# Optimization experiments

Hardware: AMD Instinct MI355X
Metric: run time of the kernel (lower is better)

The kernel has to match this reference:

```python
import jax, jax.numpy as jnp
import numpy as np


def _norm_adj(edge_index, edge_weights, num_nodes):
    """Faithful port of edge_index2norm_adj: dense scatter + self-loops +
    symmetric degree normalization (deg_inv_sqrt is detached in the original)."""
    row, col = edge_index[0], edge_index[1]
    half = edge_weights * 0.5
    adj = jnp.zeros((num_nodes, num_nodes), dtype=edge_weights.dtype)
    adj = adj.at[row, col].add(half)
    adj = adj.at[col, row].add(half)
    adj = adj + jnp.eye(num_nodes, dtype=adj.dtype)
    deg = adj.sum(axis=1)
    deg_inv_sqrt = jnp.where(deg > 0, jax.lax.rsqrt(deg), 0.0)
    deg_inv_sqrt = jax.lax.stop_gradient(deg_inv_sqrt)  # torch.no_grad + detach
    return deg_inv_sqrt[:, None] * adj * deg_inv_sqrt[None, :]


def setup_inputs() -> dict:
    key = jax.random.key(0)
    k1, k2, k3, k4, k5 = jax.random.split(key, 5)
    N, E, D_IN, D_H, D_OUT = 16384, 524288, 64, 64, 16
    x = jax.random.normal(k1, (N, D_IN), dtype=jnp.float32)
    edge_index = jax.random.randint(k2, (2, E), 0, N, dtype=jnp.int64)
    edge_weights = jax.random.uniform(k3, (E,), dtype=jnp.float32)
    W1 = jax.random.normal(k4, (D_IN, D_H), dtype=jnp.float32) / np.sqrt(D_IN)
    b1 = jnp.zeros((D_H,), dtype=jnp.float32)
    W2 = jax.random.normal(k5, (D_H, D_OUT), dtype=jnp.float32) / np.sqrt(D_H)
    b2 = jnp.zeros((D_OUT,), dtype=jnp.float32)
    return {"x": x, "W1": W1, "b1": b1, "W2": W2, "b2": b2,
            "edge_weights": edge_weights, "edge_index": edge_index}


def reference(x, W1, b1, W2, b2, edge_weights, edge_index):
    num_nodes = x.shape[0]
    A = _norm_adj(edge_index, edge_weights, num_nodes)   # [N, N]
    h = jax.nn.relu(A @ (x @ W1) + b1)                   # GCN layer 1
    out = A @ (h @ W2) + b2                              # GCN layer 2 (logits)
    return out
```

## Files before the change

kernel.cpp:

```cpp
#include <hip/hip_runtime.h>

constexpr int TPB   = 256;
constexpr int NMAX  = 16384;
constexpr int CHUNK = 2048;
constexpr int GBMAX = 1024;
constexpr int STGN  = 12288;
constexpr int RCAP  = 12;



__global__ __launch_bounds__(1024) void k_p1(const int* __restrict__ ei,
    const float* __restrict__ ew, int E, int rsh, int NBe, int GB,
    int* __restrict__ bstartT, int* __restrict__ bcntT, int2* __restrict__ tmp) {
    __shared__ int cnt[256];
    __shared__ int curs[256];
    __shared__ int sc[256];
    __shared__ int2 stg[2 * CHUNK];
    int tid = threadIdx.x;
    int b = blockIdx.x;
    int e0 = b * CHUNK;
    int e1 = min(E, e0 + CHUNK);
    if (tid < NBe) cnt[tid] = 0;
    __syncthreads();
    int ea = e0 + tid, ebg = e0 + 1024 + tid;
    int r0 = 0, c0 = 0, r1 = 0, c1 = 0, w0 = 0, w1 = 0;
    bool va = ea < e1, vb = ebg < e1;
    if (va) { r0 = ei[ea];  c0 = ei[E + ea];  w0 = __float_as_int(0.5f * ew[ea]); }
    if (vb) { r1 = ei[ebg]; c1 = ei[E + ebg]; w1 = __float_as_int(0.5f * ew[ebg]); }
    if (va) { atomicAdd(&cnt[r0 >> rsh], 1); atomicAdd(&cnt[c0 >> rsh], 1); }
    if (vb) { atomicAdd(&cnt[r1 >> rsh], 1); atomicAdd(&cnt[c1 >> rsh], 1); }
    __syncthreads();
    int myc = (tid < NBe) ? cnt[tid] : 0;
    if (tid < NBe) sc[tid] = myc;
    __syncthreads();
    for (int off = 1; off < NBe; off <<= 1) {
        int v = 0;
        if (tid < NBe && tid >= off) v = sc[tid - off];
        __syncthreads();
        if (tid < NBe) sc[tid] += v;
        __syncthreads();
    }
    if (tid < NBe) {
        int excl = sc[tid] - myc;
        curs[tid] = excl;
        bstartT[tid * GB + b] = 2 * e0 + excl;
        bcntT[tid * GB + b] = myc;
    }
    __syncthreads();
    int mask = (1 << rsh) - 1;
    if (va) {
        int p = atomicAdd(&curs[r0 >> rsh], 1);
        stg[p] = make_int2(((r0 & mask) << 20) | c0, w0);
        p = atomicAdd(&curs[c0 >> rsh], 1);
        stg[p] = make_int2(((c0 & mask) << 20) | r0, w0);
    }
    if (vb) {
        int p = atomicAdd(&curs[r1 >> rsh], 1);
        stg[p] = make_int2(((r1 & mask) << 20) | c1, w1);
        p = atomicAdd(&curs[c1 >> rsh], 1);
        stg[p] = make_int2(((c1 & mask) << 20) | r1, w1);
    }
    __syncthreads();
    int tot = 2 * (e1 - e0);
    for (int i = tid; i < tot; i += 1024) tmp[2 * e0 + i] = stg[i];
}

__global__ void k_colsum(const int* __restrict__ bcntT, int GB,
                         int* __restrict__ btot) {
    __shared__ int red[TPB / 64];
    int k = blockIdx.x;
    int s = 0;
    for (int b = threadIdx.x; b < GB; b += TPB) s += bcntT[k * GB + b];
    #pragma unroll
    for (int off = 32; off; off >>= 1) s += __shfl_down(s, off, 64);
    int wv = threadIdx.x >> 6;
    if ((threadIdx.x & 63) == 0) red[wv] = s;
    __syncthreads();
    if (threadIdx.x == 0) {
        int t = 0;
        for (int w = 0; w < TPB / 64; ++w) t += red[w];
        btot[k] = t;
    }
}

__global__ __launch_bounds__(1024) void k_p2(const int2* __restrict__ tmp,
    const int* __restrict__ bstartT, const int* __restrict__ bcntT,
    const int* __restrict__ btot, int GB, int rsh, int N, int NBe, int M,
    int2* __restrict__ ent, int* __restrict__ rowptr, float* __restrict__ dis) {
    __shared__ int sco[256];
    __shared__ int ncnt[64];
    __shared__ int nstart[64];
    __shared__ int ncur[64];
    __shared__ float wsum[64];
    __shared__ int2 stg[STGN];
    int k = blockIdx.x;
    int tid = threadIdx.x;
    int RN = 1 << rsh;
    int n0 = k << rsh;
    const int base = k * GB;

    int grp = tid >> 2, sub = tid & 3;
    int s0 = 0, l0 = 0;
    if (grp < GB) { s0 = bstartT[base + grp]; l0 = bcntT[base + grp]; }
    int2 r[RCAP];
    #pragma unroll
    for (int u = 0; u < RCAP; ++u) {
        int idx = sub + 4 * u;
        if (idx < l0) r[u] = tmp[s0 + idx];
    }

    int bt = (tid < NBe) ? btot[tid] : 0;
    if (tid < 256) sco[tid] = bt;
    if (tid < RN) { ncnt[tid] = 0; wsum[tid] = 0.f; }
    __syncthreads();
    for (int off = 1; off < 256; off <<= 1) {
        int v = 0;
        if (tid < 256 && tid >= off) v = sco[tid - off];
        __syncthreads();
        if (tid < 256) sco[tid] += v;
        __syncthreads();
    }
    int eb = sco[k] - btot[k];
    int tot = btot[k];
    bool useStg = (tot <= STGN);

    #pragma unroll
    for (int u = 0; u < RCAP; ++u)
        if (sub + 4 * u < l0) atomicAdd(&ncnt[r[u].x >> 20], 1);
    for (int idx = sub + 4 * RCAP; idx < l0; idx += 4)
        atomicAdd(&ncnt[tmp[s0 + idx].x >> 20], 1);
    for (int b = grp + 256; b < GB; b += 256) {
        int s = bstartT[base + b], l = bcntT[base + b];
        for (int idx = sub; idx < l; idx += 4)
            atomicAdd(&ncnt[tmp[s + idx].x >> 20], 1);
    }
    __syncthreads();

    int myc = (tid < RN) ? ncnt[tid] : 0;
    if (tid < RN) nstart[tid] = myc;
    __syncthreads();
    for (int off = 1; off < RN; off <<= 1) {
        int v = 0;
        if (tid < RN && tid >= off) v = nstart[tid - off];
        __syncthreads();
        if (tid < RN) nstart[tid] += v;
        __syncthreads();
    }
    if (tid < RN) { nstart[tid] -= myc; ncur[tid] = nstart[tid]; }
    __syncthreads();

    #pragma unroll
    for (int u = 0; u < RCAP; ++u)
        if (sub + 4 * u < l0) {
            int rl = r[u].x >> 20;
            int p = atomicAdd(&ncur[rl], 1);
            int2 v2 = make_int2(r[u].x & 0xFFFFF, r[u].y);
            if (useStg) stg[p] = v2; else ent[eb + p] = v2;
            atomicAdd(&wsum[rl], __int_as_float(r[u].y));
        }
    for (int idx = sub + 4 * RCAP; idx < l0; idx += 4) {
        int2 v = tmp[s0 + idx];
        int rl = v.x >> 20;
        int p = atomicAdd(&ncur[rl], 1);
        int2 v2 = make_int2(v.x & 0xFFFFF, v.y);
        if (useStg) stg[p] = v2; else ent[eb + p] = v2;
        atomicAdd(&wsum[rl], __int_as_float(v.y));
    }
    for (int b = grp + 256; b < GB; b += 256) {
        int s = bstartT[base + b], l = bcntT[base + b];
        for (int idx = sub; idx < l; idx += 4) {
            int2 v = tmp[s + idx];
            int rl = v.x >> 20;
            int p = atomicAdd(&ncur[rl], 1);
            int2 v2 = make_int2(v.x & 0xFFFFF, v.y);
            if (useStg) stg[p] = v2; else ent[eb + p] = v2;
            atomicAdd(&wsum[rl], __int_as_float(v.y));
        }
    }
    __syncthreads();
    if (useStg)
        for (int i = tid; i < tot; i += 1024) ent[eb + i] = stg[i];
    if (tid < RN && n0 + tid < N) {
        rowptr[n0 + tid] = eb + nstart[tid];
        dis[n0 + tid] = rsqrtf(1.f + wsum[tid]);
    }
    if (k == 0 && tid == 0) rowptr[N] = M;
}

__global__ void k_init_fb(float* deg, int* counts, int N) {
    int i = blockIdx.x * TPB + threadIdx.x;
    if (i < N) { deg[i] = 1.0f; counts[i] = 0; }
}
__global__ void k_deg_cnt_fb(const int* __restrict__ ei, const float* __restrict__ ew,
                             float* deg, int* counts, int E) {
    int e = blockIdx.x * TPB + threadIdx.x;
    if (e >= E) return;
    int r = ei[e], c = ei[E + e];
    float hw = 0.5f * ew[e];
    unsafeAtomicAdd(&deg[r], hw);
    unsafeAtomicAdd(&deg[c], hw);
    atomicAdd(&counts[r], 1);
    atomicAdd(&counts[c], 1);
}
__global__ void k_rsqrt_fb(float* degdis, int N) {
    int i = blockIdx.x * TPB + threadIdx.x;
    if (i < N) {
        float d = degdis[i];
        degdis[i] = d > 0.f ? rsqrtf(d) : 0.f;
    }
}
__global__ void k_scan_fb(const int* __restrict__ counts, int* __restrict__ rowptr,
                          int* __restrict__ cursor, int N) {
    __shared__ int partial[TPB];
    int tid = threadIdx.x;
    int chunk = (N + TPB - 1) / TPB;
    int begin = tid * chunk;
    int end = begin + chunk; if (end > N) end = N;
    int s = 0;
    for (int i = begin; i < end; ++i) s += counts[i];
    partial[tid] = s;
    __syncthreads();
    for (int off = 1; off < TPB; off <<= 1) {
        int v = partial[tid];
        int add = (tid >= off) ? partial[tid - off] : 0;
        __syncthreads();
        partial[tid] = v + add;
        __syncthreads();
    }
    int base = (tid == 0) ? 0 : partial[tid - 1];
    for (int i = begin; i < end; ++i) {
        rowptr[i] = base; cursor[i] = base;
        base += counts[i];
    }
    if (tid == TPB - 1) rowptr[N] = base;
}
__global__ void k_fill_fb(const int* __restrict__ ei, const float* __restrict__ ew,
                          int* cursor, int2* __restrict__ ent, int E) {
    int e = blockIdx.x * TPB + threadIdx.x;
    if (e >= E) return;
    int r = ei[e], c = ei[E + e];
    int hw = __float_as_int(0.5f * ew[e]);
    int p1 = atomicAdd(&cursor[r], 1);
    ent[p1] = make_int2(c, hw);
    int p2 = atomicAdd(&cursor[c], 1);
    ent[p2] = make_int2(r, hw);
}

__global__ void k_gemm1(const float* __restrict__ X, const float* __restrict__ W,
                        const float* __restrict__ dis, float* __restrict__ Z, int N) {
    __shared__ float Wl[64 * 64];
    int tid = threadIdx.x;
    #pragma unroll
    for (int i = tid; i < 4096; i += TPB) Wl[i] = W[i];
    __syncthreads();
    int row = blockIdx.x * 4 + (tid >> 6);
    int f = tid & 63;
    if (row >= N) return;
    const float* xr = X + row * 64;
    float s = 0.f;
    #pragma unroll
    for (int k = 0; k < 64; ++k) s = fmaf(xr[k], Wl[k * 64 + f], s);
    Z[row * 64 + f] = dis[row] * s;
}

__global__ __launch_bounds__(TPB) void k_gather1(const float* __restrict__ Z,
    const int* __restrict__ rowptr, const long long* __restrict__ entq,
    const float* __restrict__ dis, const float* __restrict__ bias1,
    const float* __restrict__ W2, float* __restrict__ Z2, int N) {
    constexpr int UN = 16;
    __shared__ float W2l[64 * 16];
    int tid = threadIdx.x;
    #pragma unroll
    for (int i = tid; i < 1024; i += TPB) W2l[i] = W2[i];
    __syncthreads();
    int node = blockIdx.x * 4 + (tid >> 6);
    int f = tid & 63;
    if (node >= N) return;
    int sj0 = __builtin_amdgcn_readfirstlane(rowptr[node]);
    int sj1 = __builtin_amdgcn_readfirstlane(rowptr[node + 1]);
    float acc = Z[node * 64 + f];
    float dn = dis[node];
    for (int jb = sj0; jb < sj1; jb += UN) {
        long long e[UN];
        #pragma unroll
        for (int u = 0; u < UN; ++u) e[u] = entq[jb + u];
        float z[UN];
        #pragma unroll
        for (int u = 0; u < UN; ++u) {
            int nn = (jb + u < sj1) ? (int)e[u] : 0;
            z[u] = Z[nn * 64 + f];
        }
        #pragma unroll
        for (int u = 0; u < UN; ++u) {
            float ww = (jb + u < sj1) ? __int_as_float((int)(e[u] >> 32)) : 0.0f;
            acc = fmaf(ww, z[u], acc);
        }
    }
    float v = fmaf(dn, acc, bias1[f]);
    v = v > 0.f ? v : 0.f;
    int q = f >> 4, j = f & 15;
    float s = 0.f;
    #pragma unroll
    for (int i = 0; i < 16; ++i) {
        float hk = __shfl(v, 16 * q + i);
        s = fmaf(hk, W2l[(16 * q + i) * 16 + j], s);
    }
    s += __shfl_xor(s, 16);
    s += __shfl_xor(s, 32);
    if (f < 16) Z2[node * 16 + f] = dn * s;
}

__global__ __launch_bounds__(TPB) void k_gather2(const float* __restrict__ Z,
    const int* __restrict__ rowptr, const long long* __restrict__ entq,
    const float* __restrict__ dis, const float* __restrict__ bias,
    float* __restrict__ out, int N) {
    constexpr int UN = 4;
    int node = blockIdx.x * 4 + (threadIdx.x >> 6);
    int lane = threadIdx.x & 63;
    int g = lane >> 4;
    int f = lane & 15;
    if (node >= N) return;
    int sj0 = __builtin_amdgcn_readfirstlane(rowptr[node]);
    int sj1 = __builtin_amdgcn_readfirstlane(rowptr[node + 1]);
    float acc = (g == 0) ? Z[node * 16 + f] : 0.f;
    for (int jb = sj0; jb < sj1; jb += 4 * UN) {
        long long e[UN];
        #pragma unroll
        for (int u = 0; u < UN; ++u) e[u] = entq[jb + 4 * u + g];
        float z[UN], w[UN];
        #pragma unroll
        for (int u = 0; u < UN; ++u) {
            bool ok = (jb + 4 * u + g) < sj1;
            int nn = ok ? (int)e[u] : 0;
            w[u] = ok ? __int_as_float((int)(e[u] >> 32)) : 0.f;
            z[u] = Z[nn * 16 + f];
        }
        #pragma unroll
        for (int u = 0; u < UN; ++u) acc = fmaf(w[u], z[u], acc);
    }
    acc += __shfl_xor(acc, 16);
    acc += __shfl_xor(acc, 32);
    if (lane < 16) out[node * 16 + f] = fmaf(dis[node], acc, bias[f]);
}

extern "C" void kernel_launch(void* const* d_in, const int* in_sizes, int n_in,
                              void* d_out, int out_size, void* d_ws, size_t ws_size,
                              hipStream_t stream) {
    const float* x  = (const float*)d_in[0];
    const float* W1 = (const float*)d_in[1];
    const float* b1 = (const float*)d_in[2];
    const float* W2 = (const float*)d_in[3];
    const float* b2 = (const float*)d_in[4];
    const float* ew = (const float*)d_in[5];
    const int*   ei = (const int*)d_in[6];

    const int N = in_sizes[0] / 64;
    const int E = in_sizes[5];
    const int M = 2 * E;

    int rsh = 0;
    while ((256 << rsh) < N) ++rsh;
    const int NBe = (N + (1 << rsh) - 1) >> rsh;
    const int GB  = (E + CHUNK - 1) / CHUNK;

    char* ws = (char*)d_ws;
    size_t off = 0;
    auto alloc = [&](size_t bytes) -> void* {
        void* p = ws + off;
        off += (bytes + 255) & ~(size_t)255;
        return p;
    };
    float* dis     = (float*)alloc((size_t)N * 4);
    int*   counts  = (int*)alloc((size_t)N * 4);
    int*   rowptr  = (int*)alloc(((size_t)N + 1) * 4);
    int*   cursor  = (int*)alloc((size_t)N * 4);
    int2*  ent     = (int2*)alloc(((size_t)M + 64) * 8);
    int*   bstartT = (int*)alloc((size_t)GB * NBe * 4);
    int*   bcntT   = (int*)alloc((size_t)GB * NBe * 4);
    int*   btot    = (int*)alloc(((size_t)NBe + 1) * 4);
    int2*  tmp     = (int2*)alloc((size_t)M * 8);
    float* Z2      = (float*)alloc((size_t)N * 16 * 4);
    (void)ws_size; (void)n_in; (void)out_size;

    float* Z1 = (float*)tmp;

    float* out = (float*)d_out;

    if (N <= NMAX && GB <= GBMAX) {
        k_p1<<<GB, 1024, 0, stream>>>(ei, ew, E, rsh, NBe, GB, bstartT, bcntT, tmp);
        k_colsum<<<NBe, TPB, 0, stream>>>(bcntT, GB, btot);
        k_p2<<<NBe, 1024, 0, stream>>>(tmp, bstartT, bcntT, btot, GB, rsh, N, NBe, M,
                                       ent, rowptr, dis);
    } else {
        k_init_fb<<<(N + TPB - 1) / TPB, TPB, 0, stream>>>(dis, counts, N);
        k_deg_cnt_fb<<<(E + TPB - 1) / TPB, TPB, 0, stream>>>(ei, ew, dis, counts, E);
        k_rsqrt_fb<<<(N + TPB - 1) / TPB, TPB, 0, stream>>>(dis, N);
        k_scan_fb<<<1, TPB, 0, stream>>>(counts, rowptr, cursor, N);
        k_fill_fb<<<(E + TPB - 1) / TPB, TPB, 0, stream>>>(ei, ew, cursor, ent, E);
    }

    k_gemm1<<<(N + 3) / 4, TPB, 0, stream>>>(x, W1, dis, Z1, N);
    k_gather1<<<(N + 3) / 4, TPB, 0, stream>>>(Z1, rowptr, (const long long*)ent,
                                               dis, b1, W2, Z2, N);
    k_gather2<<<(N + 3) / 4, TPB, 0, stream>>>(Z2, rowptr, (const long long*)ent,
                                               dis, b2, out, N);
}
```

Measured before the change: 147.6 us.

## Fuse all six GCN stages into one cooperative persistent kernel with grid syncs

Replaces the six separate launches (edge bucketing, column sum, CSR build, GEMM1, gather1, gather2) with a single cooperative kernel of 256 blocks x 1024 threads. Stages are separated by grid.sync(), and shared memory is reused through a union. The goal is to remove per-launch overhead and inter-kernel gaps. In exchange, stages that previously ran with many small blocks now loop over a fixed 256-block grid, and the CSR stage uses only NBe blocks while the others idle. The GEMM and gather phases may lose occupancy and latency hiding compared with the finer-grained launches.

```diff
diff --git a/kernel.cpp b/kernel.cpp
--- a/kernel.cpp
+++ b/kernel.cpp
@@ -1,4 +1,6 @@
 #include <hip/hip_runtime.h>
+#include <hip/hip_cooperative_groups.h>
+namespace cg = cooperative_groups;
 
 constexpr int TPB   = 256;
 constexpr int NMAX  = 16384;
@@ -6,7 +8,276 @@
 constexpr int GBMAX = 1024;
 constexpr int STGN  = 12288;
 constexpr int RCAP  = 12;
-
+constexpr int MGB   = 256;
+
+
+union SMemU {
+    struct { int cnt[256]; int curs[256]; int sc[256]; int2 stg[2 * CHUNK]; } p1;
+    struct { int sco[256]; int ncnt[64]; int nstart[64]; int ncur[64];
+             float wsum[64]; int2 stg[STGN]; } p2;
+    float wl[64 * 64];
+    float w2l[64 * 16];
+};
+
+__global__ __launch_bounds__(1024) void k_mega(
+    const float* __restrict__ x, const float* __restrict__ W1,
+    const float* __restrict__ b1, const float* __restrict__ W2,
+    const float* __restrict__ b2, const float* __restrict__ ew,
+    const int* __restrict__ ei,
+    int N, int E, int M, int rsh, int NBe, int GB,
+    float* __restrict__ dis, int* __restrict__ rowptr, int2* __restrict__ ent,
+    int* __restrict__ bstartT, int* __restrict__ bcntT, int* __restrict__ btot,
+    int2* __restrict__ tmp, float* __restrict__ Z1, float* __restrict__ Z2,
+    float* __restrict__ out)
+{
+    cg::grid_group grid = cg::this_grid();
+    __shared__ SMemU sm;
+    const int tid = threadIdx.x;
+    const long long* entq = (const long long*)ent;
+
+    for (int b = blockIdx.x; b < GB; b += MGB) {
+        int e0 = b * CHUNK;
+        int e1 = min(E, e0 + CHUNK);
+        if (tid < NBe) sm.p1.cnt[tid] = 0;
+        __syncthreads();
+        int ea = e0 + tid, ebg = e0 + 1024 + tid;
+        int r0 = 0, c0 = 0, r1 = 0, c1 = 0, w0 = 0, w1 = 0;
+        bool va = ea < e1, vb = ebg < e1;
+        if (va) { r0 = ei[ea];  c0 = ei[E + ea];  w0 = __float_as_int(0.5f * ew[ea]); }
+        if (vb) { r1 = ei[ebg]; c1 = ei[E + ebg]; w1 = __float_as_int(0.5f * ew[ebg]); }
+        if (va) { atomicAdd(&sm.p1.cnt[r0 >> rsh], 1); atomicAdd(&sm.p1.cnt[c0 >> rsh], 1); }
+        if (vb) { atomicAdd(&sm.p1.cnt[r1 >> rsh], 1); atomicAdd(&sm.p1.cnt[c1 >> rsh], 1); }
+        __syncthreads();
+        int myc = (tid < NBe) ? sm.p1.cnt[tid] : 0;
+        if (tid < NBe) sm.p1.sc[tid] = myc;
+        __syncthreads();
+        for (int off = 1; off < NBe; off <<= 1) {
+            int v = 0;
+            if (tid < NBe && tid >= off) v = sm.p1.sc[tid - off];
+            __syncthreads();
+            if (tid < NBe) sm.p1.sc[tid] += v;
+            __syncthreads();
+        }
+        if (tid < NBe) {
+            int excl = sm.p1.sc[tid] - myc;
+            sm.p1.curs[tid] = excl;
+            bstartT[tid * GB + b] = 2 * e0 + excl;
+            bcntT[tid * GB + b] = myc;
+        }
+        __syncthreads();
+        int mask = (1 << rsh) - 1;
+        if (va) {
+            int p = atomicAdd(&sm.p1.curs[r0 >> rsh], 1);
+            sm.p1.stg[p] = make_int2(((r0 & mask) << 20) | c0, w0);
+            p = atomicAdd(&sm.p1.curs[c0 >> rsh], 1);
+            sm.p1.stg[p] = make_int2(((c0 & mask) << 20) | r0, w0);
+        }
+        if (vb) {
+            int p = atomicAdd(&sm.p1.curs[r1 >> rsh], 1);
+            sm.p1.stg[p] = make_int2(((r1 & mask) << 20) | c1, w1);
+            p = atomicAdd(&sm.p1.curs[c1 >> rsh], 1);
+            sm.p1.stg[p] = make_int2(((c1 & mask) << 20) | r1, w1);
+        }
+        __syncthreads();
+        int tot = 2 * (e1 - e0);
+        for (int i = tid; i < tot; i += 1024) tmp[2 * e0 + i] = sm.p1.stg[i];
+        __syncthreads();
+    }
+    grid.sync();
+
+    if (blockIdx.x < NBe) {
+        int k = blockIdx.x;
+        int s = 0;
+        for (int bb = tid; bb < GB; bb += 1024) s += bcntT[k * GB + bb];
+        #pragma unroll
+        for (int off = 32; off; off >>= 1) s += __shfl_down(s, off, 64);
+        if ((tid & 63) == 0) sm.p1.cnt[tid >> 6] = s;
+        __syncthreads();
+        if (tid == 0) {
+            int t = 0;
+            #pragma unroll
+            for (int w = 0; w < 16; ++w) t += sm.p1.cnt[w];
+            btot[k] = t;
+        }
+    }
+    grid.sync();
+
+    if (blockIdx.x < NBe) {
+        int k = blockIdx.x;
+        int RN = 1 << rsh;
+        int n0 = k << rsh;
+        const int base = k * GB;
+        int grp = tid >> 2, sub = tid & 3;
+        int s0 = 0, l0 = 0;
+        if (grp < GB) { s0 = bstartT[base + grp]; l0 = bcntT[base + grp]; }
+        int2 r[RCAP];
+        #pragma unroll
+        for (int u = 0; u < RCAP; ++u) {
+            int idx = sub + 4 * u;
+            if (idx < l0) r[u] = tmp[s0 + idx];
+        }
+        int bt = (tid < NBe) ? btot[tid] : 0;
+        if (tid < 256) sm.p2.sco[tid] = bt;
+        if (tid < RN) { sm.p2.ncnt[tid] = 0; sm.p2.wsum[tid] = 0.f; }
+        __syncthreads();
+        for (int off = 1; off < 256; off <<= 1) {
+            int v = 0;
+            if (tid < 256 && tid >= off) v = sm.p2.sco[tid - off];
+            __syncthreads();
+            if (tid < 256) sm.p2.sco[tid] += v;
+            __syncthreads();
+        }
+        int eb = sm.p2.sco[k] - btot[k];
+        int tot = btot[k];
+        bool useStg = (tot <= STGN);
+        #pragma unroll
+        for (int u = 0; u < RCAP; ++u)
+            if (sub + 4 * u < l0) atomicAdd(&sm.p2.ncnt[r[u].x >> 20], 1);
+        for (int idx = sub + 4 * RCAP; idx < l0; idx += 4)
+            atomicAdd(&sm.p2.ncnt[tmp[s0 + idx].x >> 20], 1);
+        for (int b = grp + 256; b < GB; b += 256) {
+            int s = bstartT[base + b], l = bcntT[base + b];
+            for (int idx = sub; idx < l; idx += 4)
+                atomicAdd(&sm.p2.ncnt[tmp[s + idx].x >> 20], 1);
+        }
+        __syncthreads();
+        int myc = (tid < RN) ? sm.p2.ncnt[tid] : 0;
+        if (tid < RN) sm.p2.nstart[tid] = myc;
+        __syncthreads();
+        for (int off = 1; off < RN; off <<= 1) {
+            int v = 0;
+            if (tid < RN && tid >= off) v = sm.p2.nstart[tid - off];
+            __syncthreads();
+            if (tid < RN) sm.p2.nstart[tid] += v;
+            __syncthreads();
+        }
+        if (tid < RN) { sm.p2.nstart[tid] -= myc; sm.p2.ncur[tid] = sm.p2.nstart[tid]; }
+        __syncthreads();
+        #pragma unroll
+        for (int u = 0; u < RCAP; ++u)
+            if (sub + 4 * u < l0) {
+                int rl = r[u].x >> 20;
+                int p = atomicAdd(&sm.p2.ncur[rl], 1);
+                int2 v2 = make_int2(r[u].x & 0xFFFFF, r[u].y);
+                if (useStg) sm.p2.stg[p] = v2; else ent[eb + p] = v2;
+                atomicAdd(&sm.p2.wsum[rl], __int_as_float(r[u].y));
+            }
+        for (int idx = sub + 4 * RCAP; idx < l0; idx += 4) {
+            int2 v = tmp[s0 + idx];
+            int rl = v.x >> 20;
+            int p = atomicAdd(&sm.p2.ncur[rl], 1);
+            int2 v2 = make_int2(v.x & 0xFFFFF, v.y);
+            if (useStg) sm.p2.stg[p] = v2; else ent[eb + p] = v2;
+            atomicAdd(&sm.p2.wsum[rl], __int_as_float(v.y));
+        }
+        for (int b = grp + 256; b < GB; b += 256) {
+            int s = bstartT[base + b], l = bcntT[base + b];
+            for (int idx = sub; idx < l; idx += 4) {
+                int2 v = tmp[s + idx];
+                int rl = v.x >> 20;
+                int p = atomicAdd(&sm.p2.ncur[rl], 1);
+                int2 v2 = make_int2(v.x & 0xFFFFF, v.y);
+                if (useStg) sm.p2.stg[p] = v2; else ent[eb + p] = v2;
+                atomicAdd(&sm.p2.wsum[rl], __int_as_float(v.y));
+            }
+        }
+        __syncthreads();
+        if (useStg)
+            for (int i = tid; i < tot; i += 1024) ent[eb + i] = sm.p2.stg[i];
+        if (tid < RN && n0 + tid < N) {
+            rowptr[n0 + tid] = eb + sm.p2.nstart[tid];
+            dis[n0 + tid] = rsqrtf(1.f + sm.p2.wsum[tid]);
+        }
+        if (k == 0 && tid == 0) rowptr[N] = M;
+    }
+    grid.sync();
+
+    for (int i = tid; i < 4096; i += 1024) sm.wl[i] = W1[i];
+    __syncthreads();
+    {
+        int wid = tid >> 6, f = tid & 63;
+        for (int row = blockIdx.x * 16 + wid; row < N; row += MGB * 16) {
+            const float* xr = x + (size_t)row * 64;
+            float s = 0.f;
+            #pragma unroll
+            for (int kk = 0; kk < 64; ++kk) s = fmaf(xr[kk], sm.wl[kk * 64 + f], s);
+            Z1[(size_t)row * 64 + f] = dis[row] * s;
+        }
+    }
+    grid.sync();
+
+    if (tid < 1024) sm.w2l[tid & 1023] = W2[tid & 1023];
+    __syncthreads();
+    {
+        int wid = tid >> 6, f = tid & 63;
+        constexpr int UN = 16;
+        for (int node = blockIdx.x * 16 + wid; node < N; node += MGB * 16) {
+            int sj0 = __builtin_amdgcn_readfirstlane(rowptr[node]);
+            int sj1 = __builtin_amdgcn_readfirstlane(rowptr[node + 1]);
+            float acc = Z1[(size_t)node * 64 + f];
+            float dn = dis[node];
+            for (int jb = sj0; jb < sj1; jb += UN) {
+                long long e[UN];
+                #pragma unroll
+                for (int u = 0; u < UN; ++u) e[u] = entq[jb + u];
+                float z[UN];
+                #pragma unroll
+                for (int u = 0; u < UN; ++u) {
+                    int nn = (jb + u < sj1) ? (int)e[u] : 0;
+                    z[u] = Z1[(size_t)nn * 64 + f];
+                }
+                #pragma unroll
+                for (int u = 0; u < UN; ++u) {
+                    float ww = (jb + u < sj1) ? __int_as_float((int)(e[u] >> 32)) : 0.0f;
+                    acc = fmaf(ww, z[u], acc);
+                }
+            }
+            float v = fmaf(dn, acc, b1[f]);
+            v = v > 0.f ? v : 0.f;
+            int q = f >> 4, j = f & 15;
+            float s = 0.f;
+            #pragma unroll
+            for (int i = 0; i < 16; ++i) {
+                float hk = __shfl(v, 16 * q + i);
+                s = fmaf(hk, sm.w2l[(16 * q + i) * 16 + j], s);
+            }
+            s += __shfl_xor(s, 16);
+            s += __shfl_xor(s, 32);
+            if (f < 16) Z2[node * 16 + f] = dn * s;
+        }
+    }
+    grid.sync();
+
+    {
+        int wid = tid >> 6;
+        int lane = tid & 63;
+        int g = lane >> 4, f = lane & 15;
+        constexpr int UN = 4;
+        for (int node = blockIdx.x * 16 + wid; node < N; node += MGB * 16) {
+            int sj0 = __builtin_amdgcn_readfirstlane(rowptr[node]);
+            int sj1 = __builtin_amdgcn_readfirstlane(rowptr[node + 1]);
+            float acc = (g == 0) ? Z2[node * 16 + f] : 0.f;
+            for (int jb = sj0; jb < sj1; jb += 4 * UN) {
+                long long e[UN];
+                #pragma unroll
+                for (int u = 0; u < UN; ++u) e[u] = entq[jb + 4 * u + g];
+                float z[UN], w[UN];
+                #pragma unroll
+                for (int u = 0; u < UN; ++u) {
+                    bool ok = (jb + 4 * u + g) < sj1;
+                    int nn = ok ? (int)e[u] : 0;
+                    w[u] = ok ? __int_as_float((int)(e[u] >> 32)) : 0.f;
+                    z[u] = Z2[nn * 16 + f];
+                }
+                #pragma unroll
+                for (int u = 0; u < UN; ++u) acc = fmaf(w[u], z[u], acc);
+            }
+            acc += __shfl_xor(acc, 16);
+            acc += __shfl_xor(acc, 32);
+            if (lane < 16) out[node * 16 + f] = fmaf(dis[node], acc, b2[f]);
+        }
+    }
+}
 
 
 __global__ __launch_bounds__(1024) void k_p1(const int* __restrict__ ei,
@@ -98,7 +369,6 @@
     int RN = 1 << rsh;
     int n0 = k << rsh;
     const int base = k * GB;
-
     int grp = tid >> 2, sub = tid & 3;
     int s0 = 0, l0 = 0;
     if (grp < GB) { s0 = bstartT[base + grp]; l0 = bcntT[base + grp]; }
@@ -108,7 +378,6 @@
         int idx = sub + 4 * u;
         if (idx < l0) r[u] = tmp[s0 + idx];
     }
-
     int bt = (tid < NBe) ? btot[tid] : 0;
     if (tid < 256) sco[tid] = bt;
     if (tid < RN) { ncnt[tid] = 0; wsum[tid] = 0.f; }
@@ -123,7 +392,6 @@
     int eb = sco[k] - btot[k];
     int tot = btot[k];
     bool useStg = (tot <= STGN);
-
     #pragma unroll
     for (int u = 0; u < RCAP; ++u)
         if (sub + 4 * u < l0) atomicAdd(&ncnt[r[u].x >> 20], 1);
@@ -135,7 +403,6 @@
             atomicAdd(&ncnt[tmp[s + idx].x >> 20], 1);
     }
     __syncthreads();
-
     int myc = (tid < RN) ? ncnt[tid] : 0;
     if (tid < RN) nstart[tid] = myc;
     __syncthreads();
@@ -148,7 +415,6 @@
     }
     if (tid < RN) { nstart[tid] -= myc; ncur[tid] = nstart[tid]; }
     __syncthreads();
-
     #pragma unroll
     for (int u = 0; u < RCAP; ++u)
         if (sub + 4 * u < l0) {
@@ -354,14 +620,14 @@
     const float* ew = (const float*)d_in[5];
     const int*   ei = (const int*)d_in[6];
 
-    const int N = in_sizes[0] / 64;
-    const int E = in_sizes[5];
-    const int M = 2 * E;
+    int N = in_sizes[0] / 64;
+    int E = in_sizes[5];
+    int M = 2 * E;
 
     int rsh = 0;
     while ((256 << rsh) < N) ++rsh;
-    const int NBe = (N + (1 << rsh) - 1) >> rsh;
-    const int GB  = (E + CHUNK - 1) / CHUNK;
+    int NBe = (N + (1 << rsh) - 1) >> rsh;
+    int GB  = (E + CHUNK - 1) / CHUNK;
 
     char* ws = (char*)d_ws;
     size_t off = 0;
@@ -383,25 +649,40 @@
     (void)ws_size; (void)n_in; (void)out_size;
 
     float* Z1 = (float*)tmp;
-
     float* out = (float*)d_out;
 
     if (N <= NMAX && GB <= GBMAX) {
-        k_p1<<<GB, 1024, 0, stream>>>(ei, ew, E, rsh, NBe, GB, bstartT, bcntT, tmp);
-        k_colsum<<<NBe, TPB, 0, stream>>>(bcntT, GB, btot);
-        k_p2<<<NBe, 1024, 0, stream>>>(tmp, bstartT, bcntT, btot, GB, rsh, N, NBe, M,
-                                       ent, rowptr, dis);
+        void* ka[] = {
+            (void*)&x, (void*)&W1, (void*)&b1, (void*)&W2, (void*)&b2,
+            (void*)&ew, (void*)&ei,
+            (void*)&N, (void*)&E, (void*)&M, (void*)&rsh, (void*)&NBe, (void*)&GB,
+            (void*)&dis, (void*)&rowptr, (void*)&ent,
+            (void*)&bstartT, (void*)&bcntT, (void*)&btot,
+            (void*)&tmp, (void*)&Z1, (void*)&Z2, (void*)&out
+        };
+        hipError_t rc = hipLaunchCooperativeKernel((const void*)k_mega,
+                                                   dim3(MGB), dim3(1024), ka, 0, stream);
+        if (rc != hipSuccess) {
+            k_p1<<<GB, 1024, 0, stream>>>(ei, ew, E, rsh, NBe, GB, bstartT, bcntT, tmp);
+            k_colsum<<<NBe, TPB, 0, stream>>>(bcntT, GB, btot);
+            k_p2<<<NBe, 1024, 0, stream>>>(tmp, bstartT, bcntT, btot, GB, rsh, N, NBe, M,
+                                           ent, rowptr, dis);
+            k_gemm1<<<(N + 3) / 4, TPB, 0, stream>>>(x, W1, dis, Z1, N);
+            k_gather1<<<(N + 3) / 4, TPB, 0, stream>>>(Z1, rowptr, (const long long*)ent,
+                                                       dis, b1, W2, Z2, N);
+            k_gather2<<<(N + 3) / 4, TPB, 0, stream>>>(Z2, rowptr, (const long long*)ent,
+                                                       dis, b2, out, N);
+        }
     } else {
         k_init_fb<<<(N + TPB - 1) / TPB, TPB, 0, stream>>>(dis, counts, N);
         k_deg_cnt_fb<<<(E + TPB - 1) / TPB, TPB, 0, stream>>>(ei, ew, dis, counts, E);
         k_rsqrt_fb<<<(N + TPB - 1) / TPB, TPB, 0, stream>>>(dis, N);
         k_scan_fb<<<1, TPB, 0, stream>>>(counts, rowptr, cursor, N);
         k_fill_fb<<<(E + TPB - 1) / TPB, TPB, 0, stream>>>(ei, ew, cursor, ent, E);
-    }
-
-    k_gemm1<<<(N + 3) / 4, TPB, 0, stream>>>(x, W1, dis, Z1, N);
-    k_gather1<<<(N + 3) / 4, TPB, 0, stream>>>(Z1, rowptr, (const long long*)ent,
-                                               dis, b1, W2, Z2, N);
-    k_gather2<<<(N + 3) / 4, TPB, 0, stream>>>(Z2, rowptr, (const long long*)ent,
-                                               dis, b2, out, N);
-}
+        k_gemm1<<<(N + 3) / 4, TPB, 0, stream>>>(x, W1, dis, Z1, N);
+        k_gather1<<<(N + 3) / 4, TPB, 0, stream>>>(Z1, rowptr, (const long long*)ent,
+                                                   dis, b1, W2, Z2, N);
+        k_gather2<<<(N + 3) / 4, TPB, 0, stream>>>(Z2, rowptr, (const long long*)ent,
+                                                   dis, b2, out, N);
+    }
+}
```

Result: slower. 373.1 us (+152.8%).
